# Performance work log

Measured on AMD Instinct MI355X. Metric: run time of the kernel, lower is better.

Reference implementation:

```python
import jax, jax.numpy as jnp
import numpy as np

D_MODEL = 1024
N_HEADS = 16
D_HEAD = 64
B, S = 2, 2048


def setup_inputs() -> dict:
    key = jax.random.key(0)
    ks = jax.random.split(key, 16)
    HDH = N_HEADS * D_HEAD
    s = 0.02
    return {
        "h": jax.random.normal(ks[0], (B, S, D_MODEL), dtype=jnp.float32),
        "att_mask": jax.random.randint(ks[1], (B, S), 0, 2) > 0,
        "Wq": jax.random.normal(ks[2], (D_MODEL, HDH), dtype=jnp.float32) * s,
        "bq": jnp.zeros((HDH,), dtype=jnp.float32),
        "Wkv": jax.random.normal(ks[3], (D_MODEL, 2 * HDH), dtype=jnp.float32) * s,
        "bkv": jnp.zeros((2 * HDH,), dtype=jnp.float32),
        "Wo": jax.random.normal(ks[4], (HDH, D_MODEL), dtype=jnp.float32) * s,
        "bo": jnp.zeros((D_MODEL,), dtype=jnp.float32),
        "W1": jax.random.normal(ks[5], (D_MODEL, D_MODEL), dtype=jnp.float32) * s,
        "b1": jnp.zeros((D_MODEL,), dtype=jnp.float32),
        "W2": jax.random.normal(ks[6], (D_MODEL, D_MODEL), dtype=jnp.float32) * s,
        "b2": jnp.zeros((D_MODEL,), dtype=jnp.float32),
        "ln_g": jnp.ones((D_MODEL,), dtype=jnp.float32),
        "ln_b": jnp.zeros((D_MODEL,), dtype=jnp.float32),
    }


def _layer_norm(x, g, b, eps=1e-6):
    mu = jnp.mean(x, axis=-1, keepdims=True)
    var = jnp.mean(jnp.square(x - mu), axis=-1, keepdims=True)
    return (x - mu) * jax.lax.rsqrt(var + eps) * g + b


def reference(h, att_mask, Wq, bq, Wkv, bkv, Wo, bo, W1, b1, W2, b2, ln_g, ln_b):
    bz, ln, _ = h.shape
    scale = 1.0 / (D_HEAD ** 0.5)
    q = (h @ Wq + bq).reshape(bz, ln, N_HEADS, D_HEAD)
    kv = h @ Wkv + bkv
    k, v = jnp.split(kv, 2, axis=-1)
    k = k.reshape(bz, ln, N_HEADS, D_HEAD)
    v = v.reshape(bz, ln, N_HEADS, D_HEAD)
    # scores: [b, heads, len_q, len_k]
    scores = jnp.einsum('bqhd,bkhd->bhqk', q, k) * scale
    scores = jnp.where(att_mask[:, None, None, :], -1e9, scores)
    probs = jax.nn.softmax(scores, axis=-1)
    att = jnp.einsum('bhqk,bkhd->bqhd', probs, v).reshape(bz, ln, N_HEADS * D_HEAD)
    att_out = att @ Wo + bo
    # glu_type == 1
    g = jax.nn.sigmoid(h @ W1 + b1) * (h @ W2 + b2)
    return _layer_norm(h + att_out + g, ln_g, ln_b)
```

## Files before the change

kernel.cpp:

```cpp
#include <hip/hip_runtime.h>
#include <hip/hip_bf16.h>


typedef short bf16x8 __attribute__((ext_vector_type(8)));
typedef float f32x4  __attribute__((ext_vector_type(4)));
typedef float f32x16 __attribute__((ext_vector_type(16)));
typedef unsigned int u32x4 __attribute__((ext_vector_type(4)));

typedef const __attribute__((address_space(1))) void* gas_cvp;
typedef __attribute__((address_space(3))) void* las_vp;

__device__ __forceinline__ void gload_lds16(const void* g, void* l) {
  __builtin_amdgcn_global_load_lds((gas_cvp)g, (las_vp)l, 16, 0, 0);
}

__device__ __forceinline__ short f2bf(float f) {
  __hip_bfloat16 h = __float2bfloat16(f);
  return *reinterpret_cast<short*>(&h);
}
__device__ __forceinline__ float bf2f(short s) {
  unsigned u = ((unsigned)(unsigned short)s) << 16;
  return __builtin_bit_cast(float, u);
}

#if __has_builtin(__builtin_amdgcn_exp2f)
#define EXP2(x) __builtin_amdgcn_exp2f(x)
#else
#define EXP2(x) exp2f(x)
#endif

constexpr int BATCH = 2;
constexpr int SEQ   = 2048;
constexpr int NH    = 16;
constexpr int MROWS = BATCH * SEQ;
constexpr int NSPLIT = 2;
constexpr int KSPL   = SEQ / NSPLIT;
constexpr int RH     = MROWS * NH;


__global__ __launch_bounds__(256) void cvt_bf16(const float* __restrict__ src,
                                                short* __restrict__ dst, int n4) {
  int i = blockIdx.x * 256 + threadIdx.x;
  if (i >= n4) return;
  float4 v = reinterpret_cast<const float4*>(src)[i];
  short4 o;
  o.x = f2bf(v.x); o.y = f2bf(v.y); o.z = f2bf(v.z); o.w = f2bf(v.w);
  reinterpret_cast<short4*>(dst)[i] = o;
}

struct WtA {
  const float* s[6];
  short* d[6];
  int st[6];
  int mul[6];
  int add[6];
};
__global__ __launch_bounds__(256) void wtrans6(WtA a) {
  __shared__ float tile[32][33];
  const float* __restrict__ src = a.s[blockIdx.z];
  short* __restrict__ dst = a.d[blockIdx.z];
  const int stride = a.st[blockIdx.z];
  const int mul = a.mul[blockIdx.z], add = a.add[blockIdx.z];
  const int tx = threadIdx.x & 31, ty = threadIdx.x >> 5;
  const int n0 = blockIdx.x * 32, k0 = blockIdx.y * 32;
  #pragma unroll
  for (int i = 0; i < 32; i += 8)
    tile[ty + i][tx] = src[(size_t)(k0 + ty + i) * stride + n0 + tx];
  __syncthreads();
  #pragma unroll
  for (int i = 0; i < 32; i += 8)
    dst[(size_t)((n0 + ty + i) * mul + add) * 1024 + k0 + tx] = f2bf(tile[tx][ty + i]);
}

__global__ __launch_bounds__(256) void vtrans(const short* __restrict__ qkv,
                                              short* __restrict__ vt) {
  __shared__ short tile[32][33];
  const int tx = threadIdx.x & 31, ty = threadIdx.x >> 5;
  const int s0 = blockIdx.x * 32, d0 = blockIdx.y * 32, b = blockIdx.z;
  #pragma unroll
  for (int i = 0; i < 32; i += 8)
    tile[ty + i][tx] = qkv[(size_t)(b * SEQ + s0 + ty + i) * 3072 + 2048 + d0 + tx];
  __syncthreads();
  #pragma unroll
  for (int i = 0; i < 32; i += 8)
    vt[(size_t)(b * 1024 + d0 + ty + i) * SEQ + s0 + tx] = tile[tx][ty + i];
}

__global__ void pack_bias(const float* __restrict__ bq, const float* __restrict__ bkv,
                          const float* __restrict__ b1, const float* __restrict__ b2,
                          float* __restrict__ ball) {
  int i = blockIdx.x * 256 + threadIdx.x;
  if (i < 1024) ball[i] = bq[i];
  else if (i < 3072) ball[i] = bkv[i - 1024];
  else if (i < 4096) {
    const int j = i - 3072;
    ball[3072 + 2 * j] = b1[j];
    ball[3072 + 2 * j + 1] = b2[j];
  }
}

__device__ __forceinline__ bool mask_at(const void* mp, int idx, int flag) {
  if (flag == 1) return ((const int*)mp)[idx] != 0;
  if (flag == 2) return ((const float*)mp)[idx] != 0.f;
  return ((const unsigned char*)mp)[idx] != 0;
}

__global__ __launch_bounds__(256) void premask(const void* __restrict__ msk,
                                               float* __restrict__ mbL) {
  __shared__ int si, sf;
  const unsigned* m = (const unsigned*)msk;
  if (threadIdx.x == 0) { si = 1; sf = 1; }
  __syncthreads();
  bool oki = true, okf = true;
  for (int i = threadIdx.x; i < 1024; i += 256) {
    unsigned v = m[i];
    oki = oki && (v <= 1u);
    okf = okf && (v == 0u || v == 0x3F800000u);
  }
  if (!oki) si = 0;
  if (!okf) sf = 0;
  __syncthreads();
  const int flag = si ? 1 : (sf ? 2 : 0);
  int i = blockIdx.x * 256 + threadIdx.x;
  if (i < MROWS) mbL[i] = mask_at(msk, i, flag) ? -1.442695e9f : -8.0f;
}

template <int BN>
__global__ __launch_bounds__(256) void gemm_bf16(const short* __restrict__ A,
                                                 const short* __restrict__ BT,
                                                 const float* __restrict__ bias,
                                                 short* __restrict__ outp, int N) {
  constexpr int NF = BN / 32;
  __shared__ short Alds[4096];
  __shared__ short Blds[BN * 32];
  const int tid = threadIdx.x;
  const int w = tid >> 6, lane = tid & 63, g = lane >> 4, lr = lane & 15;
  const int wr = w >> 1, wc = w & 1;
  const int bm = blockIdx.y, bn = blockIdx.x;

  f32x4 acc[4][NF] = {};

  const int srow = tid >> 2;
  const int scol = (tid & 3) * 8;
  const short* Ab = A  + (size_t)(bm * 128 + srow) * 1024 + scol;
  const short* Bb = BT + (size_t)(bn * BN + srow) * 1024 + scol;

  for (int kt = 0; kt < 32; ++kt) {
    const int kb = kt * 32;
    __syncthreads();
    gload_lds16(Ab + kb,             &Alds[tid * 8]);
    gload_lds16(Ab + 64 * 1024 + kb, &Alds[2048 + tid * 8]);
    gload_lds16(Bb + kb,             &Blds[tid * 8]);
    if constexpr (BN == 128)
      gload_lds16(Bb + 64 * 1024 + kb, &Blds[2048 + tid * 8]);
    asm volatile("s_waitcnt vmcnt(0)" ::: "memory");
    __syncthreads();

    bf16x8 af[4], bfr[NF];
    #pragma unroll
    for (int m = 0; m < 4; ++m)
      af[m] = *reinterpret_cast<const bf16x8*>(&Alds[(wr * 64 + m * 16 + lr) * 32 + g * 8]);
    #pragma unroll
    for (int n = 0; n < NF; ++n)
      bfr[n] = *reinterpret_cast<const bf16x8*>(&Blds[(wc * (BN / 2) + n * 16 + lr) * 32 + g * 8]);
    #pragma unroll
    for (int m = 0; m < 4; ++m)
      #pragma unroll
      for (int n = 0; n < NF; ++n)
        acc[m][n] = __builtin_amdgcn_mfma_f32_16x16x32_bf16(af[m], bfr[n], acc[m][n], 0, 0, 0);
  }

  #pragma unroll
  for (int m = 0; m < 4; ++m) {
    const int row = bm * 128 + wr * 64 + m * 16 + g * 4;
    #pragma unroll
    for (int n = 0; n < NF; ++n) {
      const int col = bn * BN + wc * (BN / 2) + n * 16 + lr;
      const float bv = bias[col];
      #pragma unroll
      for (int r = 0; r < 4; ++r)
        outp[(size_t)(row + r) * N + col] = f2bf(acc[m][n][r] + bv);
    }
  }
}

__global__ __launch_bounds__(256) void gemm_qkvglu(const short* __restrict__ A,
                                                   const short* __restrict__ BT,
                                                   const float* __restrict__ bias,
                                                   short* __restrict__ qkv,
                                                   short* __restrict__ x1) {
  __shared__ short Alds[4096];
  __shared__ short Blds[4096];
  const int tid = threadIdx.x;
  const int w = tid >> 6, lane = tid & 63, g = lane >> 4, lr = lane & 15;
  const int wr = w >> 1, wc = w & 1;
  const int bm = blockIdx.y, bn = blockIdx.x;

  f32x4 acc[4][4] = {};

  const int srow = tid >> 2;
  const int scol = (tid & 3) * 8;
  const short* Ab = A  + (size_t)(bm * 128 + srow) * 1024 + scol;
  const short* Bb = BT + (size_t)(bn * 128 + srow) * 1024 + scol;

  for (int kt = 0; kt < 32; ++kt) {
    const int kb = kt * 32;
    __syncthreads();
    gload_lds16(Ab + kb,             &Alds[tid * 8]);
    gload_lds16(Ab + 64 * 1024 + kb, &Alds[2048 + tid * 8]);
    gload_lds16(Bb + kb,             &Blds[tid * 8]);
    gload_lds16(Bb + 64 * 1024 + kb, &Blds[2048 + tid * 8]);
    asm volatile("s_waitcnt vmcnt(0)" ::: "memory");
    __syncthreads();

    bf16x8 af[4], bfr[4];
    #pragma unroll
    for (int m = 0; m < 4; ++m)
      af[m] = *reinterpret_cast<const bf16x8*>(&Alds[(wr * 64 + m * 16 + lr) * 32 + g * 8]);
    #pragma unroll
    for (int n = 0; n < 4; ++n)
      bfr[n] = *reinterpret_cast<const bf16x8*>(&Blds[(wc * 64 + n * 16 + lr) * 32 + g * 8]);
    #pragma unroll
    for (int m = 0; m < 4; ++m)
      #pragma unroll
      for (int n = 0; n < 4; ++n)
        acc[m][n] = __builtin_amdgcn_mfma_f32_16x16x32_bf16(af[m], bfr[n], acc[m][n], 0, 0, 0);
  }

  const bool isGlu = (bn >= 24);
  #pragma unroll
  for (int m = 0; m < 4; ++m) {
    const int row = bm * 128 + wr * 64 + m * 16 + g * 4;
    #pragma unroll
    for (int n = 0; n < 4; ++n) {
      const int col = bn * 128 + wc * 64 + n * 16 + lr;
      const float bv = bias[col];
      #pragma unroll
      for (int r = 0; r < 4; ++r) {
        const float v = acc[m][n][r] + bv;
        if (!isGlu) {
          qkv[(size_t)(row + r) * 3072 + col] = f2bf(v);
        } else {
          const float vp = __shfl_xor(v, 1);
          if (!(lr & 1)) {
            const int col2 = col - 3072;
            x1[(size_t)(row + r) * 1024 + (col2 >> 1)] = f2bf(vp / (1.f + __expf(-v)));
          }
        }
      }
    }
  }
}

constexpr int KB = 64;
constexpr int KSLOT = 8 * 66;
constexpr int VSLOT = 8 * 66;

__global__ __launch_bounds__(256) void attn_kernel(const short* __restrict__ qkv,
                                                   const short* __restrict__ vt,
                                                   const float* __restrict__ mbL,
                                                   short* __restrict__ opart,
                                                   float* __restrict__ spart) {
  __shared__ short Kl[2][KSLOT * 8];
  __shared__ short Vl[2][VSLOT * 8];
  __shared__ float mb[KSPL];

  const int tid = threadIdx.x;
  const int w = tid >> 6, lane = tid & 63, ql = lane & 31, hi = lane >> 5;
  const int sp = blockIdx.x & (NSPLIT - 1), qb = blockIdx.x / NSPLIT;
  const int h = blockIdx.y, b = blockIdx.z;
  const int qrow = qb * 128 + w * 32 + ql;
  const int kofs = sp * KSPL;

  bf16x8 qf[4];
  {
    const short* qp = qkv + (size_t)(b * SEQ + qrow) * 3072 + h * 64;
    #pragma unroll
    for (int c = 0; c < 4; ++c)
      qf[c] = *reinterpret_cast<const bf16x8*>(qp + c * 16 + hi * 8);
  }

  const short* gkbase = qkv + (size_t)(b * SEQ + kofs) * 3072 + 1024 + h * 64
                        + (size_t)(tid >> 3) * 3072 + (tid & 7) * 8;
  const short* gvbase = vt + ((size_t)(b * 1024 + h * 64) + (tid >> 3)) * SEQ + kofs
                        + (tid & 7) * 8;
  short* kwr = &Kl[0][((tid & 7) * 66 + (tid >> 3)) * 8];
  short* vwr = &Vl[0][((tid & 7) * 66 + (tid >> 3)) * 8];

  u32x4 kreg0, kreg1, vreg0, vreg1;
  auto loadTile = [&](int kt) {
    const short* gk = gkbase + (size_t)kt * KB * 3072;
    kreg0 = *reinterpret_cast<const u32x4*>(gk);
    kreg1 = *reinterpret_cast<const u32x4*>(gk + 32 * 3072);
    const short* gv = gvbase + kt * KB;
    vreg0 = *reinterpret_cast<const u32x4*>(gv);
    vreg1 = *reinterpret_cast<const u32x4*>(gv + 32 * SEQ);
  };
  auto writeTile = [&](int buf) {
    short* kd = kwr + buf * KSLOT * 8;
    *reinterpret_cast<u32x4*>(kd)          = kreg0;
    *reinterpret_cast<u32x4*>(kd + 32 * 8) = kreg1;
    short* vd = vwr + buf * VSLOT * 8;
    *reinterpret_cast<u32x4*>(vd)          = vreg0;
    *reinterpret_cast<u32x4*>(vd + 32 * 8) = vreg1;
  };

  float s_run = 0.f;
  f32x16 oacc0 = {}, oacc1 = {};

  gload_lds16(mbL + b * SEQ + kofs + tid * 4, &mb[tid * 4]);
  loadTile(0);
  writeTile(0);
  __syncthreads();

  const short* krd = &Kl[0][(hi * 66 + ql) * 8];
  const short* vrd = &Vl[0][(hi * 66 + ql) * 8];

  constexpr int NT = KSPL / KB;
  for (int kt = 0; kt < NT; ++kt) {
    const int cur = kt & 1;
    if (kt + 1 < NT) loadTile(kt + 1);
    const short* Kb = krd + cur * KSLOT * 8;
    const short* Vb = vrd + cur * VSLOT * 8;

    #pragma unroll
    for (int t2 = 0; t2 < 2; ++t2) {
      f32x16 sc = {};
      __builtin_amdgcn_s_setprio(1);
      #pragma unroll
      for (int c = 0; c < 4; ++c) {
        bf16x8 kf = *reinterpret_cast<const bf16x8*>(Kb + (c * 132 + t2 * 32) * 8);
        sc = __builtin_amdgcn_mfma_f32_32x32x16_bf16(kf, qf[c], sc, 0, 0, 0);
      }
      __builtin_amdgcn_s_setprio(0);
      float p[16];
      #pragma unroll
      for (int u = 0; u < 4; ++u) {
        float4 m4 = *reinterpret_cast<const float4*>(&mb[kt * KB + t2 * 32 + u * 8 + hi * 4]);
        p[4 * u + 0] = EXP2(fmaf(sc[4 * u + 0], 0.18033688f, m4.x));
        p[4 * u + 1] = EXP2(fmaf(sc[4 * u + 1], 0.18033688f, m4.y));
        p[4 * u + 2] = EXP2(fmaf(sc[4 * u + 2], 0.18033688f, m4.z));
        p[4 * u + 3] = EXP2(fmaf(sc[4 * u + 3], 0.18033688f, m4.w));
      }
      {
        float a0 = (p[0] + p[1]) + (p[2] + p[3]);
        float a1 = (p[4] + p[5]) + (p[6] + p[7]);
        float a2 = (p[8] + p[9]) + (p[10] + p[11]);
        float a3 = (p[12] + p[13]) + (p[14] + p[15]);
        s_run += (a0 + a1) + (a2 + a3);
      }
      unsigned P[8];
      #pragma unroll
      for (int j = 0; j < 8; ++j)
        asm("v_cvt_pk_bf16_f32 %0, %1, %2" : "=v"(P[j]) : "v"(p[2 * j]), "v"(p[2 * j + 1]));
      asm("v_permlane32_swap_b32 %0, %1" : "+v"(P[0]), "+v"(P[2]));
      asm("v_permlane32_swap_b32 %0, %1" : "+v"(P[1]), "+v"(P[3]));
      asm("v_permlane32_swap_b32 %0, %1" : "+v"(P[4]), "+v"(P[6]));
      asm("v_permlane32_swap_b32 %0, %1" : "+v"(P[5]), "+v"(P[7]));
      u32x4 c0 = { P[0], P[1], P[2], P[3] };
      u32x4 c1 = { P[4], P[5], P[6], P[7] };
      bf16x8 pf[2] = { __builtin_bit_cast(bf16x8, c0), __builtin_bit_cast(bf16x8, c1) };

      __builtin_amdgcn_s_setprio(1);
      #pragma unroll
      for (int ch = 0; ch < 2; ++ch) {
        const int gb = (t2 * 4 + ch * 2) * 66;
        bf16x8 v0 = *reinterpret_cast<const bf16x8*>(Vb + gb * 8);
        bf16x8 v1 = *reinterpret_cast<const bf16x8*>(Vb + (gb + 32) * 8);
        oacc0 = __builtin_amdgcn_mfma_f32_32x32x16_bf16(v0, pf[ch], oacc0, 0, 0, 0);
        oacc1 = __builtin_amdgcn_mfma_f32_32x32x16_bf16(v1, pf[ch], oacc1, 0, 0, 0);
      }
      __builtin_amdgcn_s_setprio(0);
    }

    if (kt + 1 < NT) {
      writeTile(cur ^ 1);
      __syncthreads();
    }
  }

  const float sT = s_run + __shfl_xor(s_run, 32);
  const size_t obase = (size_t)sp * RH * 64 + (size_t)(b * SEQ + qrow) * 1024 + h * 64;
  #pragma unroll
  for (int dt = 0; dt < 2; ++dt) {
    #pragma unroll
    for (int u = 0; u < 4; ++u) {
      short4 st;
      const f32x16& oa = dt ? oacc1 : oacc0;
      st.x = f2bf(oa[4 * u + 0]);
      st.y = f2bf(oa[4 * u + 1]);
      st.z = f2bf(oa[4 * u + 2]);
      st.w = f2bf(oa[4 * u + 3]);
      *reinterpret_cast<short4*>(&opart[obase + dt * 32 + u * 8 + hi * 4]) = st;
    }
  }
  if (hi == 0)
    spart[sp * RH + (b * SEQ + qrow) * NH + h] = sT;
}

__global__ __launch_bounds__(256) void attn_merge(const short* __restrict__ opart,
                                                  const float* __restrict__ spart,
                                                  short* __restrict__ att) {
  const int idx = blockIdx.x * 256 + threadIdx.x;
  const int rh = idx >> 3;
  const size_t base = (size_t)rh * 64 + (idx & 7) * 8;
  float acc[8] = {};
  float ss = 0.f;
  #pragma unroll
  for (int s = 0; s < NSPLIT; ++s) {
    bf16x8 o = *reinterpret_cast<const bf16x8*>(&opart[(size_t)s * RH * 64 + base]);
    #pragma unroll
    for (int j = 0; j < 8; ++j) acc[j] += bf2f(o[j]);
    ss += spart[s * RH + rh];
  }
  const float inv = 1.f / ss;
  bf16x8 r;
  #pragma unroll
  for (int j = 0; j < 8; ++j) r[j] = f2bf(acc[j] * inv);
  *reinterpret_cast<bf16x8*>(&att[base]) = r;
}

__global__ __launch_bounds__(256) void ln_kernel(const float* __restrict__ h,
                                                 const short* __restrict__ ao,
                                                 const short* __restrict__ gl,
                                                 const float* __restrict__ gamma,
                                                 const float* __restrict__ beta,
                                                 float* __restrict__ out) {
  const int row = blockIdx.x;
  const size_t base = (size_t)row * 1024;
  const int t = threadIdx.x;
  __shared__ float red[4];
  float x[4];
  #pragma unroll
  for (int j = 0; j < 4; ++j) {
    const int c = t + j * 256;
    x[j] = h[base + c] + bf2f(ao[base + c]) + bf2f(gl[base + c]);
  }
  float s = x[0] + x[1] + x[2] + x[3];
  #pragma unroll
  for (int d = 1; d < 64; d <<= 1) s += __shfl_xor(s, d);
  if ((t & 63) == 0) red[t >> 6] = s;
  __syncthreads();
  const float mu = (red[0] + red[1] + red[2] + red[3]) * (1.f / 1024.f);
  __syncthreads();
  float vs = 0.f;
  #pragma unroll
  for (int j = 0; j < 4; ++j) { const float dx = x[j] - mu; vs += dx * dx; }
  #pragma unroll
  for (int d = 1; d < 64; d <<= 1) vs += __shfl_xor(vs, d);
  if ((t & 63) == 0) red[t >> 6] = vs;
  __syncthreads();
  const float var = (red[0] + red[1] + red[2] + red[3]) * (1.f / 1024.f);
  const float rs = rsqrtf(var + 1e-6f);
  #pragma unroll
  for (int j = 0; j < 4; ++j) {
    const int c = t + j * 256;
    out[base + c] = (x[j] - mu) * rs * gamma[c] + beta[c];
  }
}


extern "C" void kernel_launch(void* const* d_in, const int* in_sizes, int n_in,
                              void* d_out, int out_size, void* d_ws, size_t ws_size,
                              hipStream_t stream) {
  const float* h   = (const float*)d_in[0];
  const void*  msk = d_in[1];
  const float* Wq  = (const float*)d_in[2];
  const float* bq  = (const float*)d_in[3];
  const float* Wkv = (const float*)d_in[4];
  const float* bkv = (const float*)d_in[5];
  const float* Wo  = (const float*)d_in[6];
  const float* bo  = (const float*)d_in[7];
  const float* W1  = (const float*)d_in[8];
  const float* b1  = (const float*)d_in[9];
  const float* W2  = (const float*)d_in[10];
  const float* b2  = (const float*)d_in[11];
  const float* lng = (const float*)d_in[12];
  const float* lnb = (const float*)d_in[13];
  float* out = (float*)d_out;

  char* ws = (char*)d_ws;
  size_t off = 0;
  auto alloc = [&](size_t bytes) {
    char* p = ws + off;
    off += (bytes + 255) & ~(size_t)255;
    return p;
  };
  short* X     = (short*)alloc((size_t)MROWS * 1024 * 2);
  short* WALL  = (short*)alloc((size_t)5120 * 1024 * 2);
  short* WoT   = (short*)alloc((size_t)1024 * 1024 * 2);
  float* ball  = (float*)alloc(5120 * 4);
  float* MBL   = (float*)alloc((size_t)MROWS * 4);
  short* QKV   = (short*)alloc((size_t)MROWS * 3072 * 2);
  short* VT    = (short*)alloc((size_t)BATCH * 1024 * SEQ * 2);
  short* ATT   = (short*)alloc((size_t)MROWS * 1024 * 2);
  short* X1    = (short*)alloc((size_t)MROWS * 1024 * 2);
  short* AO    = (short*)alloc((size_t)MROWS * 1024 * 2);
  short* OP    = (short*)alloc((size_t)NSPLIT * RH * 64 * 2);
  float* SP    = (float*)alloc((size_t)NSPLIT * RH * 4);
  if (off > ws_size) return;

  cvt_bf16<<<4096, 256, 0, stream>>>(h, X, MROWS * 1024 / 4);
  WtA wa;
  wa.s[0] = Wq;          wa.d[0] = WALL;                wa.st[0] = 1024;  wa.mul[0] = 1; wa.add[0] = 0;
  wa.s[1] = Wkv;         wa.d[1] = WALL + 1024 * 1024;  wa.st[1] = 2048;  wa.mul[1] = 1; wa.add[1] = 0;
  wa.s[2] = Wkv + 1024;  wa.d[2] = WALL + 2048 * 1024;  wa.st[2] = 2048;  wa.mul[2] = 1; wa.add[2] = 0;
  wa.s[3] = Wo;          wa.d[3] = WoT;                 wa.st[3] = 1024;  wa.mul[3] = 1; wa.add[3] = 0;
  wa.s[4] = W1;          wa.d[4] = WALL + 3072 * 1024;  wa.st[4] = 1024;  wa.mul[4] = 2; wa.add[4] = 0;
  wa.s[5] = W2;          wa.d[5] = WALL + 3072 * 1024;  wa.st[5] = 1024;  wa.mul[5] = 2; wa.add[5] = 1;
  wtrans6<<<dim3(32, 32, 6), 256, 0, stream>>>(wa);
  pack_bias<<<16, 256, 0, stream>>>(bq, bkv, b1, b2, ball);
  premask<<<16, 256, 0, stream>>>(msk, MBL);

  gemm_qkvglu<<<dim3(40, 32), 256, 0, stream>>>(X, WALL, ball, QKV, X1);
  vtrans<<<dim3(64, 32, 2), 256, 0, stream>>>(QKV, VT);
  attn_kernel<<<dim3(16 * NSPLIT, 16, 2), 256, 0, stream>>>(QKV, VT, MBL, OP, SP);
  attn_merge<<<RH * 8 / 256, 256, 0, stream>>>(OP, SP, ATT);
  gemm_bf16<64><<<dim3(16, 32), 256, 0, stream>>>(ATT, WoT, bo, AO, 1024);
  ln_kernel<<<MROWS, 256, 0, stream>>>(h, AO, X1, lng, lnb, out);
}
```

Baseline: 175.5 us.

## Double GEMM K-tile to 64 with XOR-swizzled LDS layout

Both bf16 GEMM kernels now stage a 64-wide K slice per iteration instead of 32, halving the number of barrier/wait rounds per output tile. The LDS layout is XOR-swizzled on 16-byte chunks, with matching swizzled read addresses, to avoid bank conflicts on the fragment loads. The swizzle also permutes K elements within the 64-wide tile consistently for A and B, so the dot product is unchanged. The cost is doubled LDS usage per block, which may reduce occupancy, and the loads still do not overlap with compute.

```diff
diff --git a/kernel.cpp b/kernel.cpp
--- a/kernel.cpp
+++ b/kernel.cpp
@@ -125,56 +125,68 @@
   if (i < MROWS) mbL[i] = mask_at(msk, i, flag) ? -1.442695e9f : -8.0f;
 }
 
+
 template <int BN>
 __global__ __launch_bounds__(256) void gemm_bf16(const short* __restrict__ A,
                                                  const short* __restrict__ BT,
                                                  const float* __restrict__ bias,
                                                  short* __restrict__ outp, int N) {
-  constexpr int NF = BN / 32;
-  __shared__ short Alds[4096];
-  __shared__ short Blds[BN * 32];
+  constexpr int NF = BN / 64;
+  __shared__ short Alds[128 * 64];
+  __shared__ short Blds[BN * 64];
   const int tid = threadIdx.x;
-  const int w = tid >> 6, lane = tid & 63, g = lane >> 4, lr = lane & 15;
+  const int w = tid >> 6, l = tid & 63, lr = l & 15;
   const int wr = w >> 1, wc = w & 1;
   const int bm = blockIdx.y, bn = blockIdx.x;
 
-  f32x4 acc[4][NF] = {};
-
-  const int srow = tid >> 2;
-  const int scol = (tid & 3) * 8;
-  const short* Ab = A  + (size_t)(bm * 128 + srow) * 1024 + scol;
-  const short* Bb = BT + (size_t)(bn * BN + srow) * 1024 + scol;
-
-  for (int kt = 0; kt < 32; ++kt) {
-    const int kb = kt * 32;
+  f32x4 acc[4][2 * NF] = {};
+
+  const int srow = tid >> 3;
+  const int schunk = (tid & 7) ^ (srow & 7);
+  const short* Ab = A  + (size_t)(bm * 128 + srow) * 1024 + schunk * 8;
+  const short* Bb = BT + (size_t)(bn * BN + srow) * 1024 + schunk * 8;
+
+  const int cg = (l >> 4) ^ (l & 3), fl = (l >> 2) & 1;
+  const short* ard[2] = { &Alds[(wr * 64 + lr) * 64 + cg * 8 + fl * 32],
+                          &Alds[(wr * 64 + lr) * 64 + cg * 8 + 32 - fl * 32] };
+  const short* brd[2] = { &Blds[(wc * (BN / 2) + lr) * 64 + cg * 8 + fl * 32],
+                          &Blds[(wc * (BN / 2) + lr) * 64 + cg * 8 + 32 - fl * 32] };
+
+  for (int kt = 0; kt < 16; ++kt) {
+    const int kb = kt * 64;
     __syncthreads();
-    gload_lds16(Ab + kb,             &Alds[tid * 8]);
-    gload_lds16(Ab + 64 * 1024 + kb, &Alds[2048 + tid * 8]);
-    gload_lds16(Bb + kb,             &Blds[tid * 8]);
-    if constexpr (BN == 128)
-      gload_lds16(Bb + 64 * 1024 + kb, &Blds[2048 + tid * 8]);
+    #pragma unroll
+    for (int q = 0; q < 4; ++q)
+      gload_lds16(Ab + (size_t)q * 32 * 1024 + kb, &Alds[q * 2048 + tid * 8]);
+    #pragma unroll
+    for (int q = 0; q < BN / 32; ++q)
+      gload_lds16(Bb + (size_t)q * 32 * 1024 + kb, &Blds[q * 2048 + tid * 8]);
     asm volatile("s_waitcnt vmcnt(0)" ::: "memory");
     __syncthreads();
 
-    bf16x8 af[4], bfr[NF];
-    #pragma unroll
-    for (int m = 0; m < 4; ++m)
-      af[m] = *reinterpret_cast<const bf16x8*>(&Alds[(wr * 64 + m * 16 + lr) * 32 + g * 8]);
-    #pragma unroll
-    for (int n = 0; n < NF; ++n)
-      bfr[n] = *reinterpret_cast<const bf16x8*>(&Blds[(wc * (BN / 2) + n * 16 + lr) * 32 + g * 8]);
-    #pragma unroll
-    for (int m = 0; m < 4; ++m)
-      #pragma unroll
-      for (int n = 0; n < NF; ++n)
-        acc[m][n] = __builtin_amdgcn_mfma_f32_16x16x32_bf16(af[m], bfr[n], acc[m][n], 0, 0, 0);
-  }
-
+    #pragma unroll
+    for (int s = 0; s < 2; ++s) {
+      bf16x8 af[4], bfr[2 * NF];
+      #pragma unroll
+      for (int m = 0; m < 4; ++m)
+        af[m] = *reinterpret_cast<const bf16x8*>(ard[s] + m * 16 * 64);
+      #pragma unroll
+      for (int n = 0; n < 2 * NF; ++n)
+        bfr[n] = *reinterpret_cast<const bf16x8*>(brd[s] + n * 16 * 64);
+      #pragma unroll
+      for (int m = 0; m < 4; ++m)
+        #pragma unroll
+        for (int n = 0; n < 2 * NF; ++n)
+          acc[m][n] = __builtin_amdgcn_mfma_f32_16x16x32_bf16(af[m], bfr[n], acc[m][n], 0, 0, 0);
+    }
+  }
+
+  const int g = l >> 4;
   #pragma unroll
   for (int m = 0; m < 4; ++m) {
     const int row = bm * 128 + wr * 64 + m * 16 + g * 4;
     #pragma unroll
-    for (int n = 0; n < NF; ++n) {
+    for (int n = 0; n < 2 * NF; ++n) {
       const int col = bn * BN + wc * (BN / 2) + n * 16 + lr;
       const float bv = bias[col];
       #pragma unroll
@@ -189,44 +201,55 @@
                                                    const float* __restrict__ bias,
                                                    short* __restrict__ qkv,
                                                    short* __restrict__ x1) {
-  __shared__ short Alds[4096];
-  __shared__ short Blds[4096];
+  __shared__ short Alds[128 * 64];
+  __shared__ short Blds[128 * 64];
   const int tid = threadIdx.x;
-  const int w = tid >> 6, lane = tid & 63, g = lane >> 4, lr = lane & 15;
+  const int w = tid >> 6, l = tid & 63, lr = l & 15;
   const int wr = w >> 1, wc = w & 1;
   const int bm = blockIdx.y, bn = blockIdx.x;
 
   f32x4 acc[4][4] = {};
 
-  const int srow = tid >> 2;
-  const int scol = (tid & 3) * 8;
-  const short* Ab = A  + (size_t)(bm * 128 + srow) * 1024 + scol;
-  const short* Bb = BT + (size_t)(bn * 128 + srow) * 1024 + scol;
-
-  for (int kt = 0; kt < 32; ++kt) {
-    const int kb = kt * 32;
+  const int srow = tid >> 3;
+  const int schunk = (tid & 7) ^ (srow & 7);
+  const short* Ab = A  + (size_t)(bm * 128 + srow) * 1024 + schunk * 8;
+  const short* Bb = BT + (size_t)(bn * 128 + srow) * 1024 + schunk * 8;
+
+  const int cg = (l >> 4) ^ (l & 3), fl = (l >> 2) & 1;
+  const short* ard[2] = { &Alds[(wr * 64 + lr) * 64 + cg * 8 + fl * 32],
+                          &Alds[(wr * 64 + lr) * 64 + cg * 8 + 32 - fl * 32] };
+  const short* brd[2] = { &Blds[(wc * 64 + lr) * 64 + cg * 8 + fl * 32],
+                          &Blds[(wc * 64 + lr) * 64 + cg * 8 + 32 - fl * 32] };
+
+  for (int kt = 0; kt < 16; ++kt) {
+    const int kb = kt * 64;
     __syncthreads();
-    gload_lds16(Ab + kb,             &Alds[tid * 8]);
-    gload_lds16(Ab + 64 * 1024 + kb, &Alds[2048 + tid * 8]);
-    gload_lds16(Bb + kb,             &Blds[tid * 8]);
-    gload_lds16(Bb + 64 * 1024 + kb, &Blds[2048 + tid * 8]);
+    #pragma unroll
+    for (int q = 0; q < 4; ++q) {
+      gload_lds16(Ab + (size_t)q * 32 * 1024 + kb, &Alds[q * 2048 + tid * 8]);
+      gload_lds16(Bb + (size_t)q * 32 * 1024 + kb, &Blds[q * 2048 + tid * 8]);
+    }
     asm volatile("s_waitcnt vmcnt(0)" ::: "memory");
     __syncthreads();
 
-    bf16x8 af[4], bfr[4];
-    #pragma unroll
-    for (int m = 0; m < 4; ++m)
-      af[m] = *reinterpret_cast<const bf16x8*>(&Alds[(wr * 64 + m * 16 + lr) * 32 + g * 8]);
-    #pragma unroll
-    for (int n = 0; n < 4; ++n)
-      bfr[n] = *reinterpret_cast<const bf16x8*>(&Blds[(wc * 64 + n * 16 + lr) * 32 + g * 8]);
-    #pragma unroll
-    for (int m = 0; m < 4; ++m)
+    #pragma unroll
+    for (int s = 0; s < 2; ++s) {
+      bf16x8 af[4], bfr[4];
+      #pragma unroll
+      for (int m = 0; m < 4; ++m)
+        af[m] = *reinterpret_cast<const bf16x8*>(ard[s] + m * 16 * 64);
       #pragma unroll
       for (int n = 0; n < 4; ++n)
-        acc[m][n] = __builtin_amdgcn_mfma_f32_16x16x32_bf16(af[m], bfr[n], acc[m][n], 0, 0, 0);
-  }
-
+        bfr[n] = *reinterpret_cast<const bf16x8*>(brd[s] + n * 16 * 64);
+      #pragma unroll
+      for (int m = 0; m < 4; ++m)
+        #pragma unroll
+        for (int n = 0; n < 4; ++n)
+          acc[m][n] = __builtin_amdgcn_mfma_f32_16x16x32_bf16(af[m], bfr[n], acc[m][n], 0, 0, 0);
+    }
+  }
+
+  const int g = l >> 4;
   const bool isGlu = (bn >= 24);
   #pragma unroll
   for (int m = 0; m < 4; ++m) {
```

After: 173.2 us. About the same (-1.3%).
